# Kernel tuning notes

Measured on AMD Instinct MI355X. Metric: run time of the kernel, lower is better.

The kernel has to match this reference:

```python
import jax, jax.numpy as jnp
import numpy as np

N = 192            # image grid size (NxN)
N_SHOTS = 192
N_SAMPLES = 192
TWO_PI = 2.0 * np.pi
PIPE_ITERS = 3     # gpunufft default is ~10; 3 suffices for a CPU-runnable reference


def initialize_2D_radial(n_shots, n_samples):
    """Radial trajectory, k in [-0.5, 0.5), shape (n_shots*n_samples, 2)."""
    angles = np.pi * np.arange(n_shots) / n_shots
    radii = np.linspace(-0.5, 0.5, n_samples, endpoint=False)
    kx = radii[None, :] * np.cos(angles[:, None])
    ky = radii[None, :] * np.sin(angles[:, None])
    return np.stack([kx, ky], axis=-1).reshape(-1, 2).astype(np.float32)


def setup_inputs() -> dict:
    key = jax.random.key(0)
    x = jax.random.normal(key, (2, N, N), dtype=jnp.float32)  # real/imag image
    trajectory = jnp.asarray(initialize_2D_radial(N_SHOTS, N_SAMPLES))  # (M,2)
    return {"x": x, "trajectory": trajectory}


def _mats(traj):
    # Separable NDFT factors: exp(-2pi i k_x * px), exp(-2pi i k_y * py).
    # A: (M, N), B: (M, N); M*N complex64 ~= 57 MB each.
    p = jnp.arange(N, dtype=jnp.float32) - N / 2.0  # centered pixel coords
    A = jnp.exp(-1j * TWO_PI * traj[:, 0:1] * p[None, :])
    B = jnp.exp(-1j * TWO_PI * traj[:, 1:2] * p[None, :])
    return A.astype(jnp.complex64), B.astype(jnp.complex64)


def _op(img, A, B):
    # type-2 NUFFT (exact NDFT): image (N,N) -> kspace (M,)
    t = jnp.einsum('my,xy->mx', B, img)      # contract y first
    return jnp.einsum('mx,mx->m', A, t)


def _adj(d, A, B):
    # type-1 NUFFT adjoint: samples (M,) -> image (N,N)
    return jnp.einsum('mx,my->xy', jnp.conj(A) * d[:, None], jnp.conj(B))


def _pipe_density(A, B):
    # Pipe & Menon iterative density compensation: w <- w / |F F^H w|
    w = jnp.ones(A.shape[0], dtype=jnp.complex64)
    def body(i, w):
        q = _op(_adj(w, A, B), A, B)
        return w / jnp.maximum(jnp.abs(q), 1e-20)
    w = jax.lax.fori_loop(0, PIPE_ITERS, body, w)
    return jnp.abs(w)  # real positive weights


def reference(x, trajectory):
    img = (x[0] + 1j * x[1]).astype(jnp.complex64)  # (N,N) complex image
    A, B = _mats(trajectory)
    # density weights computed from detached trajectory (gpunufft init-time)
    traj_sg = jax.lax.stop_gradient(trajectory)
    Asg, Bsg = _mats(traj_sg)
    w = jax.lax.stop_gradient(_pipe_density(Asg, Bsg))
    kspace = _op(img, A, B)                       # forward NUFFT
    adjoint = _adj(w * kspace, A, B)              # density-compensated adjoint
    return jnp.stack([adjoint.real, adjoint.imag])  # (2,N,N) float32
```

## Files before the change

kernel.cpp:

```cpp
#include <hip/hip_runtime.h>
#include <math.h>


#define MTOT 36864
#define NPIX 192
#define SPLITS 128
#define GRP 64
#define NCH 36
#define PG 64

typedef __attribute__((ext_vector_type(8))) short s16x8;
typedef __attribute__((ext_vector_type(4))) float f32x4;
typedef __attribute__((ext_vector_type(4))) unsigned u32x4;

__device__ __forceinline__ f32x4 mfma_bf16(u32x4 a, u32x4 b, f32x4 c) {
    return __builtin_amdgcn_mfma_f32_16x16x32_bf16(
        __builtin_bit_cast(s16x8, a), __builtin_bit_cast(s16x8, b), c, 0, 0, 0);
}

__device__ __forceinline__ void g2l16(const void* g, void* l) {
    __builtin_amdgcn_global_load_lds(
        (const __attribute__((address_space(1))) void*)g,
        (__attribute__((address_space(3))) void*)l, 16, 0, 0);
}

__device__ __forceinline__ void split_pk(float a, float b, unsigned &hi, unsigned &lo) {
    const unsigned ua = __float_as_uint(a), ub = __float_as_uint(b);
    const unsigned ha = (ua + 0x8000u) & 0xffff0000u;
    const unsigned hb = (ub + 0x8000u) & 0xffff0000u;
    hi = (ha >> 16) | hb;
    const float la = a - __uint_as_float(ha);
    const float lb = b - __uint_as_float(hb);
    lo = ((__float_as_uint(la) + 0x8000u) >> 16) |
         ((__float_as_uint(lb) + 0x8000u) & 0xffff0000u);
}

__device__ __forceinline__ void ksplit(float k, float &kh, float &kl) {
    kh = __uint_as_float(__float_as_uint(k) & 0xfffff000u);
    kl = k - kh;
}
__device__ __forceinline__ float redphase(float kh, float kl, float p) {
    float r = kh * p;
    r -= rintf(r);
    r = fmaf(kl, p, r);
    return r;
}
__device__ __forceinline__ unsigned rot16(unsigned v) {
    return __builtin_amdgcn_alignbit(v, v, 16);
}
__device__ __forceinline__ int swz(int c) {
    return ((c ^ (c >> 2)) & 3) << 2;
}

__global__ void precompP_k(const float* __restrict__ traj, const int comp,
                           unsigned* __restrict__ PS) {
    const int m = blockIdx.x * 256 + threadIdx.x;
    const int c = blockIdx.y;
    float kh, kl; ksplit(traj[2 * m + comp], kh, kl);
    const float ph = redphase(kh, kl, (float)(c - 96));
    const float co = __builtin_amdgcn_cosf(ph);
    const float si = __builtin_amdgcn_sinf(ph);
    unsigned h, l; split_pk(co, -si, h, l);
    const int mc = m >> 4, mi = (m & 15) ^ swz(c);
    PS[(size_t)mc * 6144 + c * 16 + mi]        = h;
    PS[(size_t)mc * 6144 + 3072 + c * 16 + mi] = l;
}

__global__ void ebuild_k(const float* __restrict__ traj,
                         const float* __restrict__ dr, const float* __restrict__ di,
                         unsigned* __restrict__ ES) {
    const int m = blockIdx.x * 256 + threadIdx.x;
    const int c = blockIdx.y;
    float kh, kl; ksplit(traj[2 * m], kh, kl);
    const float ph = redphase(kh, kl, (float)(c - 96));
    const float co = __builtin_amdgcn_cosf(ph);
    const float si = __builtin_amdgcn_sinf(ph);
    const float dr_ = dr[m], di_ = di[m];
    const float Er = co * dr_ - si * di_;
    const float Ei = co * di_ + si * dr_;
    unsigned h, l; split_pk(Er, Ei, h, l);
    const int mc = m >> 4, mi = (m & 15) ^ swz(c);
    ES[(size_t)mc * 6144 + c * 16 + mi]        = h;
    ES[(size_t)mc * 6144 + 3072 + c * 16 + mi] = l;
}

__global__ void winit_k(float* __restrict__ wr, float* __restrict__ wi) {
    const int m = blockIdx.x * 256 + threadIdx.x;
    wr[m] = 1.f; wi[m] = 0.f;
}

__global__ __launch_bounds__(256) void adj_gemm_k(
    const unsigned* __restrict__ ES, const unsigned* __restrict__ BS,
    float* __restrict__ outP)
{
    __shared__ unsigned sAB[3][4096];
    const int tid = threadIdx.x;
    const int lane = tid & 63, wid = tid >> 6;
    const int l15 = lane & 15, qd = lane >> 4;
    const int L = blockIdx.x;
    const int xcd = L & 7, j = L >> 3;
    const int g = xcd * (GRP / 8) + j / 9;
    const int tile = j % 9;
    const int bx = tile % 3, by = tile / 3;
    const int wi = wid & 1, wj = wid >> 1;
    const int x0 = bx * 64 + wi * 32, y0 = by * 64 + wj * 32;
    float* outRe = outP + (size_t)g * (2 * MTOT);
    float* outIm = outRe + MTOT;

    f32x4 accRe[2][2], accIm[2][2];
    #pragma unroll
    for (int i = 0; i < 2; ++i)
        #pragma unroll
        for (int j2 = 0; j2 < 2; ++j2) {
            accRe[i][j2] = (f32x4){0.f, 0.f, 0.f, 0.f};
            accIm[i][j2] = (f32x4){0.f, 0.f, 0.f, 0.f};
        }

    const size_t g18 = (size_t)g * 18;
    const int exo = bx * 1024 + tid * 4;
    const int byo = by * 1024 + tid * 4;
    #define STAGE(c, buf)                                                  \
    {                                                                      \
        const size_t id_ = (g18 + (c) + (((c) >= 18) ? 1134 : 0)) * 6144; \
        const unsigned* E0_ = ES + id_;                                    \
        const unsigned* B0_ = BS + id_;                                    \
        g2l16(E0_ + exo,        &sAB[buf][tid * 4]);                       \
        g2l16(E0_ + 3072 + exo, &sAB[buf][1024 + tid * 4]);                \
        g2l16(B0_ + byo,        &sAB[buf][2048 + tid * 4]);                \
        g2l16(B0_ + 3072 + byo, &sAB[buf][3072 + tid * 4]);                \
    }

    int eoff[2], boff[2];
    #pragma unroll
    for (int t = 0; t < 2; ++t) {
        const int cE = wi * 32 + t * 16 + l15;
        eoff[t] = cE * 16 + ((qd ^ ((cE ^ (cE >> 2)) & 3)) << 2);
        const int cB = wj * 32 + t * 16 + l15;
        boff[t] = 2048 + cB * 16 + ((qd ^ ((cB ^ (cB >> 2)) & 3)) << 2);
    }

    STAGE(0, 0);
    STAGE(1, 1);

    int rb = 0;
    for (int ch = 0; ch < NCH; ++ch) {
        if (ch + 2 < NCH) {
            const int wb = (rb + 2 >= 3) ? rb - 1 : rb + 2;
            STAGE(ch + 2, wb);
            asm volatile("s_waitcnt vmcnt(8)" ::: "memory");
        } else if (ch + 1 < NCH) {
            asm volatile("s_waitcnt vmcnt(4)" ::: "memory");
        } else {
            asm volatile("s_waitcnt vmcnt(0)" ::: "memory");
        }
        __builtin_amdgcn_s_barrier();

        const unsigned* sb = &sAB[rb][0];
        u32x4 Eh[2], El[2], PhA[2], PlA[2];
        #pragma unroll
        for (int t = 0; t < 2; ++t) {
            Eh[t]  = *(const u32x4*)(sb + eoff[t]);
            El[t]  = *(const u32x4*)(sb + 1024 + eoff[t]);
            PhA[t] = *(const u32x4*)(sb + boff[t]);
            PlA[t] = *(const u32x4*)(sb + 1024 + boff[t]);
        }
        asm volatile("s_waitcnt lgkmcnt(0)" ::: "memory");
        __builtin_amdgcn_sched_barrier(0);
        __builtin_amdgcn_s_barrier();

        #pragma unroll
        for (int sj = 0; sj < 2; ++sj) {
            const u32x4 Ph = PhA[sj], Pl = PlA[sj];
            u32x4 Qh, Ql;
            #pragma unroll
            for (int r = 0; r < 4; ++r) {
                Qh[r] = rot16(Ph[r]) ^ 0x00008000u;
                Ql[r] = rot16(Pl[r]) ^ 0x00008000u;
            }
            #pragma unroll
            for (int si = 0; si < 2; ++si) {
                accRe[si][sj] = mfma_bf16(Eh[si], Ph, accRe[si][sj]);
                accRe[si][sj] = mfma_bf16(Eh[si], Pl, accRe[si][sj]);
                accRe[si][sj] = mfma_bf16(El[si], Ph, accRe[si][sj]);
                accIm[si][sj] = mfma_bf16(Eh[si], Qh, accIm[si][sj]);
                accIm[si][sj] = mfma_bf16(Eh[si], Ql, accIm[si][sj]);
                accIm[si][sj] = mfma_bf16(El[si], Qh, accIm[si][sj]);
            }
        }
        rb = (rb + 1 == 3) ? 0 : rb + 1;
    }
    #undef STAGE

    #pragma unroll
    for (int si = 0; si < 2; ++si)
        #pragma unroll
        for (int sj = 0; sj < 2; ++sj)
            #pragma unroll
            for (int rg = 0; rg < 4; ++rg) {
                const int x = x0 + si * 16 + qd * 4 + rg;
                const int y = y0 + sj * 16 + l15;
                outRe[x * NPIX + y] = accRe[si][sj][rg];
                outIm[x * NPIX + y] = accIm[si][sj][rg];
            }
}

__device__ __forceinline__ void fw_stage_load(const unsigned* __restrict__ Ghi,
                                              const unsigned* __restrict__ Glo,
                                              int tid, int koff, u32x4 st[3]) {
    #pragma unroll
    for (int j = 0; j < 3; ++j) {
        const int li = tid + j * 576;
        if (li < 1536) {
            const int row = li >> 3, pl = (li >> 2) & 1, qt = li & 3;
            const unsigned* src = pl ? Glo : Ghi;
            st[j] = *(const u32x4*)(src + row * 192 + koff + qt * 4);
        }
    }
}
__device__ __forceinline__ void fw_stage_write(unsigned* sb, int tid, const u32x4 st[3]) {
    #pragma unroll
    for (int j = 0; j < 3; ++j) {
        const int li = tid + j * 576;
        if (li < 1536) {
            const int row = li >> 3, pl = (li >> 2) & 1, qt = li & 3;
            *(u32x4*)(sb + pl * 3840 + row * 20 + qt * 4) = st[j];
        }
    }
}

__global__ __launch_bounds__(576) void fwdq_k(
    const float* __restrict__ traj,
    const unsigned* __restrict__ Ghi, const unsigned* __restrict__ Glo,
    float* __restrict__ wre, float* __restrict__ wim,
    const int mode,
    float* __restrict__ qre, float* __restrict__ qim)
{
    __shared__ unsigned sG[2][2 * 3840];
    const int tid = threadIdx.x;
    const int lane = tid & 63, wid = tid >> 6;
    const int l15 = lane & 15, q = lane >> 4;
    const int m = (blockIdx.x * 9 + wid) * 16 + l15;
    const float2 kk = *(const float2*)(traj + 2 * m);
    float kxh, kxl, kyh, kyl;
    ksplit(kk.x, kxh, kxl);
    ksplit(kk.y, kyh, kyl);

    f32x4 tre[12], tim[12];
    #pragma unroll
    for (int i = 0; i < 12; ++i) {
        tre[i] = (f32x4){0.f, 0.f, 0.f, 0.f};
        tim[i] = (f32x4){0.f, 0.f, 0.f, 0.f};
    }

    float bc, bs;
    { const float ph = redphase(kyh, kyl, (float)(q * 4 - 96)); 
      bc = __builtin_amdgcn_cosf(ph); bs = __builtin_amdgcn_sinf(ph); }
    const float r1c = __builtin_amdgcn_cosf(kk.y), r1s = __builtin_amdgcn_sinf(kk.y);
    float r16c, r16s;
    { float g = kk.y * 16.f; g -= rintf(g);
      r16c = __builtin_amdgcn_cosf(g); r16s = __builtin_amdgcn_sinf(g); }

    u32x4 st[3];
    fw_stage_load(Ghi, Glo, tid, 0, st);
    fw_stage_write(&sG[0][0], tid, st);
    __syncthreads();

    for (int ch = 0; ch < 12; ++ch) {
        if (ch < 11) fw_stage_load(Ghi, Glo, tid, (ch + 1) * 16, st);

        u32x4 Ph, Pl, Qh, Ql;
        {
            float c = bc, s = bs;
            #pragma unroll
            for (int r = 0; r < 4; ++r) {
                unsigned h, l; split_pk(c, s, h, l);
                Ph[r] = h; Pl[r] = l;
                Qh[r] = rot16(h) ^ 0x00008000u;
                Ql[r] = rot16(l) ^ 0x00008000u;
                const float nc = c * r1c - s * r1s, ns = s * r1c + c * r1s;
                c = nc; s = ns;
            }
            const float nbc = bc * r16c - bs * r16s, nbs = bs * r16c + bc * r16s;
            bc = nbc; bs = nbs;
        }

        const unsigned* sb = &sG[ch & 1][0];
        #pragma unroll
        for (int si = 0; si < 12; ++si) {
            const int base = (si * 16 + l15) * 20 + q * 4;
            const u32x4 gh = *(const u32x4*)(sb + base);
            const u32x4 gl = *(const u32x4*)(sb + 3840 + base);
            tre[si] = mfma_bf16(gh, Ph, tre[si]);
            tre[si] = mfma_bf16(gh, Pl, tre[si]);
            tre[si] = mfma_bf16(gl, Ph, tre[si]);
            tim[si] = mfma_bf16(gh, Qh, tim[si]);
            tim[si] = mfma_bf16(gh, Ql, tim[si]);
            tim[si] = mfma_bf16(gl, Qh, tim[si]);
        }

        if (ch < 11) {
            __syncthreads();
            fw_stage_write(&sG[(ch + 1) & 1][0], tid, st);
            __syncthreads();
        }
    }

    float qr = 0.f, qi = 0.f;
    {
        float g = kk.x * 16.f; g -= rintf(g);
        const float rc = __builtin_amdgcn_cosf(g), rs = __builtin_amdgcn_sinf(g);
        #pragma unroll
        for (int rg = 0; rg < 4; ++rg) {
            const float ph = redphase(kxh, kxl, (float)(q * 4 + rg - 96));
            float c = __builtin_amdgcn_cosf(ph), s = __builtin_amdgcn_sinf(ph);
            #pragma unroll
            for (int si = 0; si < 12; ++si) {
                const float tr = tre[si][rg], ti = tim[si][rg];
                qr += c * tr + s * ti;
                qi += c * ti - s * tr;
                const float nc = c * rc - s * rs, ns = s * rc + c * rs;
                c = nc; s = ns;
            }
        }
    }
    qr += __shfl_xor(qr, 16); qi += __shfl_xor(qi, 16);
    qr += __shfl_xor(qr, 32); qi += __shfl_xor(qi, 32);
    if (lane < 16) {
        if (mode == 0) {
            const float den = fmaxf(sqrtf(qr * qr + qi * qi), 1e-20f);
            wre[m] /= den; wim[m] /= den;
        } else {
            const float sc = sqrtf(wre[m] * wre[m] + wim[m] * wim[m]);
            qre[m] = qr * sc; qim[m] = qi * sc;
        }
    }
}

__global__ void presplit_k(const float* __restrict__ re, const float* __restrict__ im,
                           unsigned* __restrict__ Gh, unsigned* __restrict__ Gl) {
    const int e = blockIdx.x * 256 + threadIdx.x;
    unsigned h, l;
    split_pk(re[e], im[e], h, l);
    Gh[e] = h; Gl[e] = l;
}

__global__ void presplitP_k(const float* __restrict__ outP,
                            unsigned* __restrict__ Gh, unsigned* __restrict__ Gl) {
    const int e = blockIdx.x * 256 + threadIdx.x;
    float re = 0.f, im = 0.f;
    #pragma unroll 8
    for (int g = 0; g < PG; ++g) {
        re += outP[(size_t)g * (2 * MTOT) + e];
        im += outP[(size_t)g * (2 * MTOT) + MTOT + e];
    }
    unsigned h, l;
    split_pk(re, im, h, l);
    Gh[e] = h; Gl[e] = l;
}

__global__ void reduceOut_k(const float* __restrict__ outP, float* __restrict__ out) {
    const int e = blockIdx.x * 256 + threadIdx.x;
    float re = 0.f, im = 0.f;
    #pragma unroll 8
    for (int g = 0; g < PG; ++g) {
        re += outP[(size_t)g * (2 * MTOT) + e];
        im += outP[(size_t)g * (2 * MTOT) + MTOT + e];
    }
    out[e] = re; out[MTOT + e] = im;
}

extern "C" void kernel_launch(void* const* d_in, const int* in_sizes, int n_in,
                              void* d_out, int out_size, void* d_ws, size_t ws_size,
                              hipStream_t stream)
{
    const float* xin  = (const float*)d_in[0];
    const float* traj = (const float*)d_in[1];
    float* out = (float*)d_out;

    char* pb = (char*)d_ws;
    unsigned* BS = (unsigned*)pb; pb += (size_t)2304 * 6144 * 4;
    unsigned* ES = (unsigned*)pb; pb += (size_t)2304 * 6144 * 4;
    float* outP = (float*)pb; pb += (size_t)PG * 2 * MTOT * 4;
    float* wr   = (float*)pb; pb += MTOT * 4;
    float* wi   = (float*)pb; pb += MTOT * 4;
    float* dre  = (float*)pb; pb += MTOT * 4;
    float* dim_ = (float*)pb; pb += MTOT * 4;
    unsigned* Ghi = (unsigned*)pb; pb += MTOT * 4;
    unsigned* Glo = (unsigned*)pb; pb += MTOT * 4;

    precompP_k<<<dim3(MTOT / 256, NPIX), 256, 0, stream>>>(traj, 1, BS);
    winit_k<<<MTOT / 256, 256, 0, stream>>>(wr, wi);

    for (int it = 0; it < 3; ++it) {
        ebuild_k<<<dim3(MTOT / 256, NPIX), 256, 0, stream>>>(traj, wr, wi, ES);
        adj_gemm_k<<<9 * GRP, 256, 0, stream>>>(ES, BS, outP);
        presplitP_k<<<MTOT / 256, 256, 0, stream>>>(outP, Ghi, Glo);
        fwdq_k<<<256, 576, 0, stream>>>(traj, Ghi, Glo, wr, wi, 0, dre, dim_);
    }

    presplit_k<<<MTOT / 256, 256, 0, stream>>>(xin, xin + MTOT, Ghi, Glo);
    fwdq_k<<<256, 576, 0, stream>>>(traj, Ghi, Glo, wr, wi, 1, dre, dim_);
    ebuild_k<<<dim3(MTOT / 256, NPIX), 256, 0, stream>>>(traj, dre, dim_, ES);
    adj_gemm_k<<<9 * GRP, 256, 0, stream>>>(ES, BS, outP);
    reduceOut_k<<<MTOT / 256, 256, 0, stream>>>(outP, out);
}
```

Before: 463.2 us.

## Double adjoint split count and read forward operand directly from global memory

The adjoint GEMM now splits the sample dimension into 128 groups of 18 chunks each, replacing 64 groups of 36 chunks with an irregular chunk index mapping. This doubles the grid size and the partial-output buffer, which should improve occupancy across CUs at the cost of a larger reduction. The forward kernel drops its LDS double-buffered staging and barriers and loads the hi/lo image operands straight from global memory (L2-resident) into MFMA registers. That removes synchronisation but risks uncoalesced or repeated global loads.

```diff
diff --git a/kernel.cpp b/kernel.cpp
--- a/kernel.cpp
+++ b/kernel.cpp
@@ -5,9 +5,9 @@
 #define MTOT 36864
 #define NPIX 192
 #define SPLITS 128
-#define GRP 64
-#define NCH 36
-#define PG 64
+#define MPS (MTOT / SPLITS)
+#define ADJ_CHUNKS (MPS / 16)
+#define PG 128
 
 typedef __attribute__((ext_vector_type(8))) short s16x8;
 typedef __attribute__((ext_vector_type(4))) float f32x4;
@@ -99,12 +99,12 @@
     const int l15 = lane & 15, qd = lane >> 4;
     const int L = blockIdx.x;
     const int xcd = L & 7, j = L >> 3;
-    const int g = xcd * (GRP / 8) + j / 9;
+    const int s = xcd * (SPLITS / 8) + j / 9;
     const int tile = j % 9;
     const int bx = tile % 3, by = tile / 3;
     const int wi = wid & 1, wj = wid >> 1;
     const int x0 = bx * 64 + wi * 32, y0 = by * 64 + wj * 32;
-    float* outRe = outP + (size_t)g * (2 * MTOT);
+    float* outRe = outP + (size_t)s * (2 * MTOT);
     float* outIm = outRe + MTOT;
 
     f32x4 accRe[2][2], accIm[2][2];
@@ -116,12 +116,12 @@
             accIm[i][j2] = (f32x4){0.f, 0.f, 0.f, 0.f};
         }
 
-    const size_t g18 = (size_t)g * 18;
+    const size_t s18 = (size_t)s * ADJ_CHUNKS;
     const int exo = bx * 1024 + tid * 4;
     const int byo = by * 1024 + tid * 4;
     #define STAGE(c, buf)                                                  \
     {                                                                      \
-        const size_t id_ = (g18 + (c) + (((c) >= 18) ? 1134 : 0)) * 6144; \
+        const size_t id_ = (s18 + (c)) * 6144;                             \
         const unsigned* E0_ = ES + id_;                                    \
         const unsigned* B0_ = BS + id_;                                    \
         g2l16(E0_ + exo,        &sAB[buf][tid * 4]);                       \
@@ -143,12 +143,12 @@
     STAGE(1, 1);
 
     int rb = 0;
-    for (int ch = 0; ch < NCH; ++ch) {
-        if (ch + 2 < NCH) {
+    for (int ch = 0; ch < ADJ_CHUNKS; ++ch) {
+        if (ch + 2 < ADJ_CHUNKS) {
             const int wb = (rb + 2 >= 3) ? rb - 1 : rb + 2;
             STAGE(ch + 2, wb);
             asm volatile("s_waitcnt vmcnt(8)" ::: "memory");
-        } else if (ch + 1 < NCH) {
+        } else if (ch + 1 < ADJ_CHUNKS) {
             asm volatile("s_waitcnt vmcnt(4)" ::: "memory");
         } else {
             asm volatile("s_waitcnt vmcnt(0)" ::: "memory");
@@ -204,30 +204,6 @@
             }
 }
 
-__device__ __forceinline__ void fw_stage_load(const unsigned* __restrict__ Ghi,
-                                              const unsigned* __restrict__ Glo,
-                                              int tid, int koff, u32x4 st[3]) {
-    #pragma unroll
-    for (int j = 0; j < 3; ++j) {
-        const int li = tid + j * 576;
-        if (li < 1536) {
-            const int row = li >> 3, pl = (li >> 2) & 1, qt = li & 3;
-            const unsigned* src = pl ? Glo : Ghi;
-            st[j] = *(const u32x4*)(src + row * 192 + koff + qt * 4);
-        }
-    }
-}
-__device__ __forceinline__ void fw_stage_write(unsigned* sb, int tid, const u32x4 st[3]) {
-    #pragma unroll
-    for (int j = 0; j < 3; ++j) {
-        const int li = tid + j * 576;
-        if (li < 1536) {
-            const int row = li >> 3, pl = (li >> 2) & 1, qt = li & 3;
-            *(u32x4*)(sb + pl * 3840 + row * 20 + qt * 4) = st[j];
-        }
-    }
-}
-
 __global__ __launch_bounds__(576) void fwdq_k(
     const float* __restrict__ traj,
     const unsigned* __restrict__ Ghi, const unsigned* __restrict__ Glo,
@@ -235,7 +211,6 @@
     const int mode,
     float* __restrict__ qre, float* __restrict__ qim)
 {
-    __shared__ unsigned sG[2][2 * 3840];
     const int tid = threadIdx.x;
     const int lane = tid & 63, wid = tid >> 6;
     const int l15 = lane & 15, q = lane >> 4;
@@ -260,14 +235,9 @@
     { float g = kk.y * 16.f; g -= rintf(g);
       r16c = __builtin_amdgcn_cosf(g); r16s = __builtin_amdgcn_sinf(g); }
 
-    u32x4 st[3];
-    fw_stage_load(Ghi, Glo, tid, 0, st);
-    fw_stage_write(&sG[0][0], tid, st);
-    __syncthreads();
+    const int lanebase = l15 * NPIX + q * 4;
 
     for (int ch = 0; ch < 12; ++ch) {
-        if (ch < 11) fw_stage_load(Ghi, Glo, tid, (ch + 1) * 16, st);
-
         u32x4 Ph, Pl, Qh, Ql;
         {
             float c = bc, s = bs;
@@ -284,24 +254,18 @@
             bc = nbc; bs = nbs;
         }
 
-        const unsigned* sb = &sG[ch & 1][0];
+        const int cb = lanebase + ch * 16;
         #pragma unroll
         for (int si = 0; si < 12; ++si) {
-            const int base = (si * 16 + l15) * 20 + q * 4;
-            const u32x4 gh = *(const u32x4*)(sb + base);
-            const u32x4 gl = *(const u32x4*)(sb + 3840 + base);
+            const int base = si * (16 * NPIX) + cb;
+            const u32x4 gh = *(const u32x4*)(Ghi + base);
+            const u32x4 gl = *(const u32x4*)(Glo + base);
             tre[si] = mfma_bf16(gh, Ph, tre[si]);
             tre[si] = mfma_bf16(gh, Pl, tre[si]);
             tre[si] = mfma_bf16(gl, Ph, tre[si]);
             tim[si] = mfma_bf16(gh, Qh, tim[si]);
             tim[si] = mfma_bf16(gh, Ql, tim[si]);
             tim[si] = mfma_bf16(gl, Qh, tim[si]);
-        }
-
-        if (ch < 11) {
-            __syncthreads();
-            fw_stage_write(&sG[(ch + 1) & 1][0], tid, st);
-            __syncthreads();
         }
     }
 
@@ -393,7 +357,7 @@
 
     for (int it = 0; it < 3; ++it) {
         ebuild_k<<<dim3(MTOT / 256, NPIX), 256, 0, stream>>>(traj, wr, wi, ES);
-        adj_gemm_k<<<9 * GRP, 256, 0, stream>>>(ES, BS, outP);
+        adj_gemm_k<<<9 * SPLITS, 256, 0, stream>>>(ES, BS, outP);
         presplitP_k<<<MTOT / 256, 256, 0, stream>>>(outP, Ghi, Glo);
         fwdq_k<<<256, 576, 0, stream>>>(traj, Ghi, Glo, wr, wi, 0, dre, dim_);
     }
@@ -401,6 +365,6 @@
     presplit_k<<<MTOT / 256, 256, 0, stream>>>(xin, xin + MTOT, Ghi, Glo);
     fwdq_k<<<256, 576, 0, stream>>>(traj, Ghi, Glo, wr, wi, 1, dre, dim_);
     ebuild_k<<<dim3(MTOT / 256, NPIX), 256, 0, stream>>>(traj, dre, dim_, ES);
-    adj_gemm_k<<<9 * GRP, 256, 0, stream>>>(ES, BS, outP);
+    adj_gemm_k<<<9 * SPLITS, 256, 0, stream>>>(ES, BS, outP);
     reduceOut_k<<<MTOT / 256, 256, 0, stream>>>(outP, out);
 }
```

After: 685.8 us. +48.1%, slower.

## Pre-swizzle image chunks and stream them to LDS with direct global loads

Applied to the files above, without the earlier changes.

The presplit kernels now write the hi/lo bf16 image planes in a chunked, XOR-swizzled layout so that each 16-column chunk is contiguous. The forward kernel loads these chunks straight into LDS with global_load_lds, replacing the register-staged copy and dropping one barrier per chunk. It also changes to 256-thread blocks with 4 waves instead of 576 threads with 9 waves, launching 576 blocks. The intent is to cut LDS staging overhead and bank conflicts, but the fwdq kernel is only a small share of the total pipeline time.

```diff
diff --git a/kernel.cpp b/kernel.cpp
--- a/kernel.cpp
+++ b/kernel.cpp
@@ -204,42 +204,18 @@
             }
 }
 
-__device__ __forceinline__ void fw_stage_load(const unsigned* __restrict__ Ghi,
-                                              const unsigned* __restrict__ Glo,
-                                              int tid, int koff, u32x4 st[3]) {
-    #pragma unroll
-    for (int j = 0; j < 3; ++j) {
-        const int li = tid + j * 576;
-        if (li < 1536) {
-            const int row = li >> 3, pl = (li >> 2) & 1, qt = li & 3;
-            const unsigned* src = pl ? Glo : Ghi;
-            st[j] = *(const u32x4*)(src + row * 192 + koff + qt * 4);
-        }
-    }
-}
-__device__ __forceinline__ void fw_stage_write(unsigned* sb, int tid, const u32x4 st[3]) {
-    #pragma unroll
-    for (int j = 0; j < 3; ++j) {
-        const int li = tid + j * 576;
-        if (li < 1536) {
-            const int row = li >> 3, pl = (li >> 2) & 1, qt = li & 3;
-            *(u32x4*)(sb + pl * 3840 + row * 20 + qt * 4) = st[j];
-        }
-    }
-}
-
-__global__ __launch_bounds__(576) void fwdq_k(
+__global__ __launch_bounds__(256) void fwdq_k(
     const float* __restrict__ traj,
     const unsigned* __restrict__ Ghi, const unsigned* __restrict__ Glo,
     float* __restrict__ wre, float* __restrict__ wim,
     const int mode,
     float* __restrict__ qre, float* __restrict__ qim)
 {
-    __shared__ unsigned sG[2][2 * 3840];
+    __shared__ unsigned sG[2][6144];
     const int tid = threadIdx.x;
     const int lane = tid & 63, wid = tid >> 6;
     const int l15 = lane & 15, q = lane >> 4;
-    const int m = (blockIdx.x * 9 + wid) * 16 + l15;
+    const int m = (blockIdx.x * 4 + wid) * 16 + l15;
     const float2 kk = *(const float2*)(traj + 2 * m);
     float kxh, kxl, kyh, kyl;
     ksplit(kk.x, kxh, kxl);
@@ -253,20 +229,37 @@
     }
 
     float bc, bs;
-    { const float ph = redphase(kyh, kyl, (float)(q * 4 - 96)); 
+    { const float ph = redphase(kyh, kyl, (float)(q * 4 - 96));
       bc = __builtin_amdgcn_cosf(ph); bs = __builtin_amdgcn_sinf(ph); }
     const float r1c = __builtin_amdgcn_cosf(kk.y), r1s = __builtin_amdgcn_sinf(kk.y);
     float r16c, r16s;
     { float g = kk.y * 16.f; g -= rintf(g);
       r16c = __builtin_amdgcn_cosf(g); r16s = __builtin_amdgcn_sinf(g); }
 
-    u32x4 st[3];
-    fw_stage_load(Ghi, Glo, tid, 0, st);
-    fw_stage_write(&sG[0][0], tid, st);
+    int goff[12];
+    #pragma unroll
+    for (int si = 0; si < 12; ++si) {
+        const int row = si * 16 + l15;
+        goff[si] = row * 16 + ((q ^ ((row ^ (row >> 2)) & 3)) << 2);
+    }
+
+    #define FSTAGE(c, buf)                                                     \
+    {                                                                          \
+        const int cb_ = (c) * 3072;                                            \
+        _Pragma("unroll")                                                      \
+        for (int v = 0; v < 3; ++v) {                                          \
+            g2l16(Ghi + cb_ + v * 1024 + tid * 4,                              \
+                  &sG[buf][v * 1024 + tid * 4]);                               \
+            g2l16(Glo + cb_ + v * 1024 + tid * 4,                              \
+                  &sG[buf][3072 + v * 1024 + tid * 4]);                        \
+        }                                                                      \
+    }
+
+    FSTAGE(0, 0);
     __syncthreads();
 
     for (int ch = 0; ch < 12; ++ch) {
-        if (ch < 11) fw_stage_load(Ghi, Glo, tid, (ch + 1) * 16, st);
+        if (ch < 11) FSTAGE(ch + 1, (ch + 1) & 1);
 
         u32x4 Ph, Pl, Qh, Ql;
         {
@@ -287,9 +280,8 @@
         const unsigned* sb = &sG[ch & 1][0];
         #pragma unroll
         for (int si = 0; si < 12; ++si) {
-            const int base = (si * 16 + l15) * 20 + q * 4;
-            const u32x4 gh = *(const u32x4*)(sb + base);
-            const u32x4 gl = *(const u32x4*)(sb + 3840 + base);
+            const u32x4 gh = *(const u32x4*)(sb + goff[si]);
+            const u32x4 gl = *(const u32x4*)(sb + 3072 + goff[si]);
             tre[si] = mfma_bf16(gh, Ph, tre[si]);
             tre[si] = mfma_bf16(gh, Pl, tre[si]);
             tre[si] = mfma_bf16(gl, Ph, tre[si]);
@@ -298,12 +290,9 @@
             tim[si] = mfma_bf16(gl, Qh, tim[si]);
         }
 
-        if (ch < 11) {
-            __syncthreads();
-            fw_stage_write(&sG[(ch + 1) & 1][0], tid, st);
-            __syncthreads();
-        }
-    }
+        if (ch < 11) __syncthreads();
+    }
+    #undef FSTAGE
 
     float qr = 0.f, qi = 0.f;
     {
@@ -341,7 +330,9 @@
     const int e = blockIdx.x * 256 + threadIdx.x;
     unsigned h, l;
     split_pk(re[e], im[e], h, l);
-    Gh[e] = h; Gl[e] = l;
+    const int x = e / NPIX, y = e % NPIX;
+    const int o = (y >> 4) * 3072 + x * 16 + ((y & 15) ^ swz(x));
+    Gh[o] = h; Gl[o] = l;
 }
 
 __global__ void presplitP_k(const float* __restrict__ outP,
@@ -355,7 +346,9 @@
     }
     unsigned h, l;
     split_pk(re, im, h, l);
-    Gh[e] = h; Gl[e] = l;
+    const int x = e / NPIX, y = e % NPIX;
+    const int o = (y >> 4) * 3072 + x * 16 + ((y & 15) ^ swz(x));
+    Gh[o] = h; Gl[o] = l;
 }
 
 __global__ void reduceOut_k(const float* __restrict__ outP, float* __restrict__ out) {
@@ -395,11 +388,11 @@
         ebuild_k<<<dim3(MTOT / 256, NPIX), 256, 0, stream>>>(traj, wr, wi, ES);
         adj_gemm_k<<<9 * GRP, 256, 0, stream>>>(ES, BS, outP);
         presplitP_k<<<MTOT / 256, 256, 0, stream>>>(outP, Ghi, Glo);
-        fwdq_k<<<256, 576, 0, stream>>>(traj, Ghi, Glo, wr, wi, 0, dre, dim_);
+        fwdq_k<<<576, 256, 0, stream>>>(traj, Ghi, Glo, wr, wi, 0, dre, dim_);
     }
 
     presplit_k<<<MTOT / 256, 256, 0, stream>>>(xin, xin + MTOT, Ghi, Glo);
-    fwdq_k<<<256, 576, 0, stream>>>(traj, Ghi, Glo, wr, wi, 1, dre, dim_);
+    fwdq_k<<<576, 256, 0, stream>>>(traj, Ghi, Glo, wr, wi, 1, dre, dim_);
     ebuild_k<<<dim3(MTOT / 256, NPIX), 256, 0, stream>>>(traj, dre, dim_, ES);
     adj_gemm_k<<<9 * GRP, 256, 0, stream>>>(ES, BS, outP);
     reduceOut_k<<<MTOT / 256, 256, 0, stream>>>(outP, out);
```

Measured after the change: 504.9 us. 1.09x slower.

## Fuse E-matrix construction into adjoint GEMM, drop ebuild kernel and ES buffer

Applied to the files above, without the earlier changes.

The weighted phase matrix E is no longer precomputed into a large global buffer by a separate kernel. The adjoint GEMM now loads trajectory and weights for its sample group into LDS and computes the E tiles (sin/cos, complex multiply, bf16 hi/lo split) on the fly into a double-buffered LDS slot, while B tiles are still streamed asynchronously. This removes a roughly 56 MB write plus re-read per adjoint call and four kernel launches, in exchange for extra transcendental ALU work interleaved with the MFMA loop (recomputed by each of the 9 tiles per group). It also drops one __syncthreads before the staging write in the forward kernel.

```diff
diff --git a/kernel.cpp b/kernel.cpp
--- a/kernel.cpp
+++ b/kernel.cpp
@@ -66,34 +66,19 @@
     PS[(size_t)mc * 6144 + 3072 + c * 16 + mi] = l;
 }
 
-__global__ void ebuild_k(const float* __restrict__ traj,
-                         const float* __restrict__ dr, const float* __restrict__ di,
-                         unsigned* __restrict__ ES) {
-    const int m = blockIdx.x * 256 + threadIdx.x;
-    const int c = blockIdx.y;
-    float kh, kl; ksplit(traj[2 * m], kh, kl);
-    const float ph = redphase(kh, kl, (float)(c - 96));
-    const float co = __builtin_amdgcn_cosf(ph);
-    const float si = __builtin_amdgcn_sinf(ph);
-    const float dr_ = dr[m], di_ = di[m];
-    const float Er = co * dr_ - si * di_;
-    const float Ei = co * di_ + si * dr_;
-    unsigned h, l; split_pk(Er, Ei, h, l);
-    const int mc = m >> 4, mi = (m & 15) ^ swz(c);
-    ES[(size_t)mc * 6144 + c * 16 + mi]        = h;
-    ES[(size_t)mc * 6144 + 3072 + c * 16 + mi] = l;
-}
-
 __global__ void winit_k(float* __restrict__ wr, float* __restrict__ wi) {
     const int m = blockIdx.x * 256 + threadIdx.x;
     wr[m] = 1.f; wi[m] = 0.f;
 }
 
 __global__ __launch_bounds__(256) void adj_gemm_k(
-    const unsigned* __restrict__ ES, const unsigned* __restrict__ BS,
-    float* __restrict__ outP)
+    const float* __restrict__ traj,
+    const float* __restrict__ dr_g, const float* __restrict__ di_g,
+    const unsigned* __restrict__ BS, float* __restrict__ outP)
 {
-    __shared__ unsigned sAB[3][4096];
+    __shared__ unsigned sE[2][2048];
+    __shared__ unsigned sB[3][2048];
+    __shared__ float kxA[576], drA[576], diA[576];
     const int tid = threadIdx.x;
     const int lane = tid & 63, wid = tid >> 6;
     const int l15 = lane & 15, qd = lane >> 4;
@@ -107,6 +92,18 @@
     float* outRe = outP + (size_t)g * (2 * MTOT);
     float* outIm = outRe + MTOT;
 
+    #pragma unroll
+    for (int rep = 0; rep < 3; ++rep) {
+        const int idx = tid + rep * 256;
+        if (idx < 576) {
+            const int mg = (idx < 288) ? g * 288 + idx
+                                       : (g + 64) * 288 + (idx - 288);
+            kxA[idx] = traj[2 * mg];
+            drA[idx] = dr_g[mg];
+            diA[idx] = di_g[mg];
+        }
+    }
+
     f32x4 accRe[2][2], accIm[2][2];
     #pragma unroll
     for (int i = 0; i < 2; ++i)
@@ -116,18 +113,41 @@
             accIm[i][j2] = (f32x4){0.f, 0.f, 0.f, 0.f};
         }
 
+    const int cE_ = tid >> 2;
+    const float pf = (float)(bx * 64 + cE_ - 96);
+    const int miq = tid & 3;
+    const int ewaddr = cE_ * 16 + ((miq ^ ((cE_ ^ (cE_ >> 2)) & 3)) << 2);
+
+    #define ECOMP(c, eb)                                                   \
+    {                                                                      \
+        const int db = (c) * 16 + miq * 4;                                 \
+        const f32x4 kx4 = *(const f32x4*)(kxA + db);                       \
+        const f32x4 dr4 = *(const f32x4*)(drA + db);                       \
+        const f32x4 di4 = *(const f32x4*)(diA + db);                       \
+        u32x4 hv, lv;                                                      \
+        _Pragma("unroll")                                                  \
+        for (int jj = 0; jj < 4; ++jj) {                                   \
+            float kh_, kl_; ksplit(kx4[jj], kh_, kl_);                     \
+            const float ph_ = redphase(kh_, kl_, pf);                      \
+            const float co_ = __builtin_amdgcn_cosf(ph_);                  \
+            const float si_ = __builtin_amdgcn_sinf(ph_);                  \
+            const float Er_ = co_ * dr4[jj] - si_ * di4[jj];               \
+            const float Ei_ = co_ * di4[jj] + si_ * dr4[jj];               \
+            unsigned h_, l_; split_pk(Er_, Ei_, h_, l_);                   \
+            hv[jj] = h_; lv[jj] = l_;                                      \
+        }                                                                  \
+        *(u32x4*)(&sE[eb][ewaddr])        = hv;                            \
+        *(u32x4*)(&sE[eb][1024 + ewaddr]) = lv;                            \
+    }
+
     const size_t g18 = (size_t)g * 18;
-    const int exo = bx * 1024 + tid * 4;
     const int byo = by * 1024 + tid * 4;
-    #define STAGE(c, buf)                                                  \
+    #define STAGEB(c, buf)                                                 \
     {                                                                      \
         const size_t id_ = (g18 + (c) + (((c) >= 18) ? 1134 : 0)) * 6144; \
-        const unsigned* E0_ = ES + id_;                                    \
         const unsigned* B0_ = BS + id_;                                    \
-        g2l16(E0_ + exo,        &sAB[buf][tid * 4]);                       \
-        g2l16(E0_ + 3072 + exo, &sAB[buf][1024 + tid * 4]);                \
-        g2l16(B0_ + byo,        &sAB[buf][2048 + tid * 4]);                \
-        g2l16(B0_ + 3072 + byo, &sAB[buf][3072 + tid * 4]);                \
+        g2l16(B0_ + byo,        &sB[buf][tid * 4]);                        \
+        g2l16(B0_ + 3072 + byo, &sB[buf][1024 + tid * 4]);                 \
     }
 
     int eoff[2], boff[2];
@@ -136,31 +156,37 @@
         const int cE = wi * 32 + t * 16 + l15;
         eoff[t] = cE * 16 + ((qd ^ ((cE ^ (cE >> 2)) & 3)) << 2);
         const int cB = wj * 32 + t * 16 + l15;
-        boff[t] = 2048 + cB * 16 + ((qd ^ ((cB ^ (cB >> 2)) & 3)) << 2);
-    }
-
-    STAGE(0, 0);
-    STAGE(1, 1);
-
-    int rb = 0;
+        boff[t] = cB * 16 + ((qd ^ ((cB ^ (cB >> 2)) & 3)) << 2);
+    }
+
+    STAGEB(0, 0);
+    STAGEB(1, 1);
+    __syncthreads();
+    ECOMP(0, 0);
+    asm volatile("s_waitcnt lgkmcnt(0)" ::: "memory");
+
     for (int ch = 0; ch < NCH; ++ch) {
         if (ch + 2 < NCH) {
-            const int wb = (rb + 2 >= 3) ? rb - 1 : rb + 2;
-            STAGE(ch + 2, wb);
-            asm volatile("s_waitcnt vmcnt(8)" ::: "memory");
+            const int rb3 = ch % 3;
+            const int wb = (rb3 + 2 >= 3) ? rb3 - 1 : rb3 + 2;
+            STAGEB(ch + 2, wb);
+            asm volatile("s_waitcnt vmcnt(4)" ::: "memory");
         } else if (ch + 1 < NCH) {
-            asm volatile("s_waitcnt vmcnt(4)" ::: "memory");
+            asm volatile("s_waitcnt vmcnt(2)" ::: "memory");
         } else {
             asm volatile("s_waitcnt vmcnt(0)" ::: "memory");
         }
         __builtin_amdgcn_s_barrier();
 
-        const unsigned* sb = &sAB[rb][0];
+        if (ch + 1 < NCH) ECOMP(ch + 1, (ch + 1) & 1);
+
+        const unsigned* se = &sE[ch & 1][0];
+        const unsigned* sb = &sB[ch % 3][0];
         u32x4 Eh[2], El[2], PhA[2], PlA[2];
         #pragma unroll
         for (int t = 0; t < 2; ++t) {
-            Eh[t]  = *(const u32x4*)(sb + eoff[t]);
-            El[t]  = *(const u32x4*)(sb + 1024 + eoff[t]);
+            Eh[t]  = *(const u32x4*)(se + eoff[t]);
+            El[t]  = *(const u32x4*)(se + 1024 + eoff[t]);
             PhA[t] = *(const u32x4*)(sb + boff[t]);
             PlA[t] = *(const u32x4*)(sb + 1024 + boff[t]);
         }
@@ -187,9 +213,9 @@
                 accIm[si][sj] = mfma_bf16(El[si], Qh, accIm[si][sj]);
             }
         }
-        rb = (rb + 1 == 3) ? 0 : rb + 1;
-    }
-    #undef STAGE
+    }
+    #undef ECOMP
+    #undef STAGEB
 
     #pragma unroll
     for (int si = 0; si < 2; ++si)
@@ -299,7 +325,6 @@
         }
 
         if (ch < 11) {
-            __syncthreads();
             fw_stage_write(&sG[(ch + 1) & 1][0], tid, st);
             __syncthreads();
         }
@@ -379,7 +404,6 @@
 
     char* pb = (char*)d_ws;
     unsigned* BS = (unsigned*)pb; pb += (size_t)2304 * 6144 * 4;
-    unsigned* ES = (unsigned*)pb; pb += (size_t)2304 * 6144 * 4;
     float* outP = (float*)pb; pb += (size_t)PG * 2 * MTOT * 4;
     float* wr   = (float*)pb; pb += MTOT * 4;
     float* wi   = (float*)pb; pb += MTOT * 4;
@@ -392,15 +416,13 @@
     winit_k<<<MTOT / 256, 256, 0, stream>>>(wr, wi);
 
     for (int it = 0; it < 3; ++it) {
-        ebuild_k<<<dim3(MTOT / 256, NPIX), 256, 0, stream>>>(traj, wr, wi, ES);
-        adj_gemm_k<<<9 * GRP, 256, 0, stream>>>(ES, BS, outP);
+        adj_gemm_k<<<9 * GRP, 256, 0, stream>>>(traj, wr, wi, BS, outP);
         presplitP_k<<<MTOT / 256, 256, 0, stream>>>(outP, Ghi, Glo);
         fwdq_k<<<256, 576, 0, stream>>>(traj, Ghi, Glo, wr, wi, 0, dre, dim_);
     }
 
     presplit_k<<<MTOT / 256, 256, 0, stream>>>(xin, xin + MTOT, Ghi, Glo);
     fwdq_k<<<256, 576, 0, stream>>>(traj, Ghi, Glo, wr, wi, 1, dre, dim_);
-    ebuild_k<<<dim3(MTOT / 256, NPIX), 256, 0, stream>>>(traj, dre, dim_, ES);
-    adj_gemm_k<<<9 * GRP, 256, 0, stream>>>(ES, BS, outP);
+    adj_gemm_k<<<9 * GRP, 256, 0, stream>>>(traj, dre, dim_, BS, outP);
     reduceOut_k<<<MTOT / 256, 256, 0, stream>>>(outP, out);
 }
```

After: 457.7 us. About the same (-1.2%).
